# Performance work log

Measured on AMD Instinct MI355X. Metric: run time of the kernel, lower is better.

## Reference

```python
import jax, jax.numpy as jnp
import numpy as np

HEAD = 4
HW_DIM = 256  # in_dim // 2


def _gconv1x1(x, w, b):
    # groups=2 pointwise conv: x [B,C,H,W], w [O, C//2], b [O]
    B, C, H, W = x.shape
    O = w.shape[0]
    xg = x.reshape(B, 2, C // 2, H, W)
    wg = w.reshape(2, O // 2, C // 2)
    y = jnp.einsum('bgchw,goc->bgohw', xg, wg).reshape(B, O, H, W)
    return y + b[None, :, None, None]


def _bn_train(x, w, b, eps=1e-5):
    # BatchNorm2d in training mode (batch statistics over N,H,W)
    mean = x.mean(axis=(0, 2, 3), keepdims=True)
    var = ((x - mean) ** 2).mean(axis=(0, 2, 3), keepdims=True)
    return (x - mean) / jnp.sqrt(var + eps) * w[None, :, None, None] + b[None, :, None, None]


def _forward(x, wq, bq, wk, bk, wv, bv, bnh_w, bnh_b, bnw_w, bnw_b, gamma):
    B, C, H, W = x.shape
    org_x = x
    # first half of channels is detached in the original forward
    xd = jnp.concatenate([jax.lax.stop_gradient(x[:, :HW_DIM]), x[:, HW_DIM:]], axis=1)

    dqk_h = 512 // HEAD  # 128 per-head qk dim == `long`
    dv_h = 256 // HEAD   # 64 per-head value dim
    q = _gconv1x1(xd, wq, bq).reshape(B, HEAD, dqk_h, H, W)
    k = _gconv1x1(xd, wk, bk).reshape(B, HEAD, dqk_h, H, W)
    v = _gconv1x1(xd, wv, bv).reshape(B, HEAD, dv_h, H, W)
    scale = dqk_h ** (-0.5)

    # --- attention along H (per width column) ---
    eH = jnp.einsum('bnciw,bncjw->bnwij', q, k) * scale  # [B,HEAD,W,H,H]
    aH = jax.nn.softmax(eH, axis=-1)
    out_H = jnp.einsum('bnwij,bncjw->bnciw', aH, v).reshape(B, HEAD * dv_h, H, W)

    # --- attention along W (per height row) ---
    eW = jnp.einsum('bnchi,bnchj->bnhij', q, k) * scale  # [B,HEAD,H,W,W]
    aW = jax.nn.softmax(eW, axis=-1)
    out_W = jnp.einsum('bnhij,bnchj->bnchi', aW, v).reshape(B, HEAD * dv_h, H, W)

    p0 = _bn_train(out_H, bnh_w, bnh_b)[:, :HW_DIM // 2]
    p1 = _bn_train(out_W, bnw_w, bnw_b)[:, :HW_DIM // 2]

    out_temp = jnp.concatenate([out_H, out_W], axis=1)  # pre-BN outputs
    out = gamma * jax.nn.relu(out_temp) + org_x
    return out, p0, p1


def setup_inputs() -> dict:
    key = jax.random.key(0)
    ks = jax.random.split(key, 4)
    B, C, H, W = 4, 512, 128, 128
    s = 0.02
    return {
        'x': jax.random.normal(ks[0], (B, C, H, W), jnp.float32),
        'wq': jax.random.normal(ks[1], (512, 256), jnp.float32) * s,
        'bq': jnp.zeros((512,), jnp.float32),
        'wk': jax.random.normal(ks[2], (512, 256), jnp.float32) * s,
        'bk': jnp.zeros((512,), jnp.float32),
        'wv': jax.random.normal(ks[3], (256, 256), jnp.float32) * s,
        'bv': jnp.zeros((256,), jnp.float32),
        'bnh_w': jnp.ones((256,), jnp.float32),
        'bnh_b': jnp.zeros((256,), jnp.float32),
        'bnw_w': jnp.ones((256,), jnp.float32),
        'bnw_b': jnp.zeros((256,), jnp.float32),
        'gamma': jnp.full((1,), 0.1, jnp.float32),
    }


def reference(x, wq, bq, wk, bk, wv, bv, bnh_w, bnh_b, bnw_w, bnw_b, gamma):
    return _forward(x, wq, bq, wk, bk, wv, bv, bnh_w, bnh_b, bnw_w, bnw_b, gamma)
```

## Files before the change

### kernel.cpp

```cpp
#include <hip/hip_runtime.h>
#include <cstdint>
#include <cstddef>

constexpr int Bn = 4, Cin = 512, Hn = 128, Wn = 128, HWn = Hn * Wn;
constexpr float SCALE_LOG2E = 0.12751743f;
constexpr float INV_CNT = 1.52587890625e-05f;

typedef unsigned short u16;
typedef unsigned int u32;
using f32x4  = __attribute__((ext_vector_type(4))) float;
using bf16x8 = __attribute__((ext_vector_type(8))) short;

#define MFMA(a, b, c) __builtin_amdgcn_mfma_f32_16x16x32_bf16((a), (b), (c), 0, 0, 0)

__device__ __forceinline__ u16 bfu(float f) {
  u32 u = __float_as_uint(f);
  u += 0x7fffu + ((u >> 16) & 1u);
  return (u16)(u >> 16);
}

__device__ __forceinline__ void gload_lds16(const void* g, void* l) {
  __builtin_amdgcn_global_load_lds(
      (const __attribute__((address_space(1))) u32*)g,
      (__attribute__((address_space(3))) u32*)l, 16, 0, 0);
}

constexpr size_t SZ_XT = (size_t)Bn * HWn * 512 * 2;
constexpr size_t SZ_QK = (size_t)Bn * 4 * HWn * 128 * 2;
constexpr size_t SZ_V  = (size_t)Bn * 4 * HWn * 64 * 2;
constexpr size_t SZ_O  = (size_t)Bn * 256 * HWn * 4;
constexpr size_t OFF_XT = 0;
constexpr size_t OFF_Q  = OFF_XT + SZ_XT;
constexpr size_t OFF_K  = OFF_Q + SZ_QK;
constexpr size_t OFF_V  = OFF_K + SZ_QK;
constexpr size_t OFF_OH = OFF_V + SZ_V;
constexpr size_t OFF_OW = OFF_OH + SZ_O;
constexpr size_t OFF_ST = OFF_OW + SZ_O;
constexpr size_t OFF_WB = OFF_ST + 4096;
constexpr size_t OFF_BB = OFF_WB + (size_t)1280 * 256 * 2;

__global__ __launch_bounds__(256) void k_transpose_cast(
    const float* __restrict__ x,
    const float* __restrict__ wq, const float* __restrict__ wk, const float* __restrict__ wv,
    const float* __restrict__ bq, const float* __restrict__ bk, const float* __restrict__ bv,
    u16* __restrict__ xT, u16* __restrict__ Wb, float* __restrict__ Bb) {
  __shared__ float tile[32][33];
  const int t = threadIdx.x;
  if (blockIdx.z == 4) {
    if (blockIdx.y == 0 && blockIdx.x < 320) {
      int idx = (blockIdx.x * 256 + t) * 4;
      int row = idx >> 8, col = idx & 255;
      const float* src = (row < 512)  ? (wq + (size_t)row * 256 + col)
                       : (row < 1024) ? (wk + (size_t)(row - 512) * 256 + col)
                                      : (wv + (size_t)(row - 1024) * 256 + col);
      float4 v = *(const float4*)src;
      u32 lo = (u32)bfu(v.x) | ((u32)bfu(v.y) << 16);
      u32 hi = (u32)bfu(v.z) | ((u32)bfu(v.w) << 16);
      *(uint2*)&Wb[idx] = make_uint2(lo, hi);
    } else if (blockIdx.y == 1 && blockIdx.x == 0) {
      for (int i = t; i < 1280; i += 256)
        Bb[i] = (i < 512) ? bq[i] : (i < 1024) ? bk[i - 512] : bv[i - 1024];
    }
    return;
  }
  const int b = blockIdx.z, c0 = blockIdx.y * 32, p0 = blockIdx.x * 32;
  const int pi = t & 31, ci = t >> 5;
  const float* xp = x + ((size_t)b * Cin + c0) * HWn + p0;
  for (int cc = ci; cc < 32; cc += 8) tile[cc][pi] = xp[(size_t)cc * HWn + pi];
  __syncthreads();
  u16* o = xT + ((size_t)b * HWn + p0) * Cin + c0;
  for (int pp = ci; pp < 32; pp += 8) o[(size_t)pp * Cin + pi] = bfu(tile[pi][pp]);
}

__global__ __launch_bounds__(256, 3) void k_proj(
    const u16* __restrict__ xT, const u16* __restrict__ Wb, const float* __restrict__ Bb,
    u16* __restrict__ Q, u16* __restrict__ K, u16* __restrict__ V,
    float* __restrict__ stats) {
  __shared__ u16 xs[128 * 128];

  const int t = threadIdx.x;
  const int flat = blockIdx.x + 10 * (blockIdx.y + (blockIdx.z << 7));
  const int work = ((flat & 7) * 640) + (flat >> 3);
  const int ot = work % 10;
  const int rest = work / 10;
  const int b = rest >> 7;
  const int pos0 = (rest & 127) << 7;

  if (work == 0) { stats[t] = 0.f; stats[256 + t] = 0.f; }

  const int g = (ot < 8) ? ((ot & 3) >> 1) : (ot - 8);
  const u16* xrow = xT + ((size_t)b * HWn + pos0) * 512 + g * 256;

  const int lane = t & 63, wid = t >> 6, ln = lane & 15, qd = lane >> 4;
  const u16* wr0 = Wb + ((size_t)ot * 128 + wid * 32 + ln) * 256;

  f32x4 acc[2][8];
#pragma unroll
  for (int mi = 0; mi < 2; ++mi)
#pragma unroll
    for (int nt = 0; nt < 8; ++nt) acc[mi][nt] = f32x4{0.f, 0.f, 0.f, 0.f};

  for (int kc = 0; kc < 2; ++kc) {
    __syncthreads();
#pragma unroll
    for (int p = 0; p < 8; ++p) {
      int id = p * 256 + t;
      int pos = id >> 4, kb = id & 15;
      gload_lds16(xrow + (size_t)pos * 512 + kc * 128 + ((kb ^ (pos & 15)) << 3),
                  xs + id * 8);
    }
    bf16x8 a[2][4];
#pragma unroll
    for (int kk = 0; kk < 4; ++kk) {
      int kbi = kk * 4 + qd;
      a[0][kk] = *(const bf16x8*)(wr0 + kc * 128 + kbi * 8);
      a[1][kk] = *(const bf16x8*)(wr0 + 16 * 256 + kc * 128 + kbi * 8);
    }
    __syncthreads();
#pragma unroll
    for (int kk = 0; kk < 4; ++kk) {
      int kbi = kk * 4 + qd;
#pragma unroll
      for (int nt = 0; nt < 8; ++nt) {
        bf16x8 bf_ = *(const bf16x8*)(xs + (nt * 16 + ln) * 128 + (kbi ^ ln) * 8);
        acc[0][nt] = MFMA(a[0][kk], bf_, acc[0][nt]);
        acc[1][nt] = MFMA(a[1][kk], bf_, acc[1][nt]);
      }
    }
  }
  __syncthreads();
#pragma unroll
  for (int mi = 0; mi < 2; ++mi) {
    int oc = wid * 32 + mi * 16 + qd * 4;
    const float* bp = Bb + ot * 128 + oc;
    float b0 = bp[0], b1 = bp[1], b2 = bp[2], b3 = bp[3];
    int ocb = oc >> 2;
#pragma unroll
    for (int nt = 0; nt < 8; ++nt) {
      int pos = nt * 16 + ln;
      u32 lo = (u32)bfu(acc[mi][nt][0] + b0) | ((u32)bfu(acc[mi][nt][1] + b1) << 16);
      u32 hi = (u32)bfu(acc[mi][nt][2] + b2) | ((u32)bfu(acc[mi][nt][3] + b3) << 16);
      *(uint2*)&xs[pos * 128 + ((ocb ^ (pos & 31)) << 2)] = make_uint2(lo, hi);
    }
  }
  __syncthreads();
  if (ot < 8) {
    u16* dst = (ot < 4) ? Q + (size_t)(b * 4 + ot) * HWn * 128
                        : K + (size_t)(b * 4 + (ot - 4)) * HWn * 128;
#pragma unroll
    for (int p = 0; p < 8; ++p) {
      int id = p * 256 + t;
      int pos = id >> 4, grp = id & 15;
      int s0 = (grp * 2) ^ (pos & 31), s1 = (grp * 2 + 1) ^ (pos & 31);
      uint2 g0 = *(const uint2*)&xs[pos * 128 + (s0 << 2)];
      uint2 g1 = *(const uint2*)&xs[pos * 128 + (s1 << 2)];
      *(uint4*)(dst + (size_t)(pos0 + pos) * 128 + grp * 8) = make_uint4(g0.x, g0.y, g1.x, g1.y);
    }
  } else {
    u16* vb = V + (size_t)(b * 4 + (ot - 8) * 2) * HWn * 64;
#pragma unroll
    for (int p = 0; p < 8; ++p) {
      int id = p * 256 + t;
      int pos = id >> 4, grp = id & 15;
      int off = grp * 8;
      int s0 = (grp * 2) ^ (pos & 31), s1 = (grp * 2 + 1) ^ (pos & 31);
      uint2 g0 = *(const uint2*)&xs[pos * 128 + (s0 << 2)];
      uint2 g1 = *(const uint2*)&xs[pos * 128 + (s1 << 2)];
      u16* d = vb + (size_t)((off >> 6) * HWn + pos0 + pos) * 64 + (off & 63);
      *(uint4*)d = make_uint4(g0.x, g0.y, g1.x, g1.y);
    }
  }
}

__global__ __launch_bounds__(256, 3) void k_attn(
    const u16* __restrict__ Qg, const u16* __restrict__ Kg, const u16* __restrict__ Vg,
    const float* __restrict__ x, const float* __restrict__ gamma,
    float* __restrict__ outH, float* __restrict__ oWraw, float* __restrict__ out,
    float* __restrict__ stats) {
  __shared__ u16 sm[64 * 128 + 128 * 128];
  u16* VT = sm;
  u16* KP = sm + 64 * 128;
  float* scr = (float*)sm;

  const int t = threadIdx.x;
  const int s = blockIdx.x;
  const int b = blockIdx.y >> 2, n = blockIdx.y & 3;
  const int dir = blockIdx.z;
  const int pos_base = (dir == 0) ? s : s * 128;
  const int step = (dir == 0) ? 128 : 1;

  const u16* qb = Qg + (size_t)(b * 4 + n) * HWn * 128;
  const u16* kb = Kg + (size_t)(b * 4 + n) * HWn * 128;
  const u16* vb = Vg + (size_t)(b * 4 + n) * HWn * 64;

  const int lane = t & 63, wid = t >> 6, ln = lane & 15, qd = lane >> 4;

#pragma unroll
  for (int p = 0; p < 8; ++p) {
    int id = p * 256 + t;
    int row = id >> 4, kk = id & 15;
    gload_lds16(kb + (size_t)(pos_base + row * step) * 128 + ((kk ^ (row & 15)) << 3),
                KP + id * 8);
  }
  uint4 vreg[4];
#pragma unroll
  for (int p = 0; p < 4; ++p) {
    int id = p * 256 + t;
    int j = id >> 3, cb = id & 7;
    vreg[p] = *(const uint4*)(vb + (size_t)(pos_base + j * step) * 64 + cb * 8);
  }
  bf16x8 qa[2][4];
#pragma unroll
  for (int kk = 0; kk < 4; ++kk) {
    int kbi = kk * 4 + qd;
    qa[0][kk] = *(const bf16x8*)(qb + (size_t)(pos_base + (wid * 32 + ln) * step) * 128 + kbi * 8);
    qa[1][kk] = *(const bf16x8*)(qb + (size_t)(pos_base + (wid * 32 + 16 + ln) * step) * 128 + kbi * 8);
  }
#pragma unroll
  for (int p = 0; p < 4; ++p) {
    int id = p * 256 + t;
    int j = id >> 3, cb = id & 7;
    const u16* pv = (const u16*)&vreg[p];
    int jb = j >> 3, jr = j & 7;
#pragma unroll
    for (int e = 0; e < 8; ++e) {
      int c = cb * 8 + e;
      int sc = ((c >> 3) ^ c) & 15;
      VT[c * 128 + ((((jb ^ sc) & 15) << 3) | jr)] = pv[e];
    }
  }
  __syncthreads();

  f32x4 accS[2][8];
#pragma unroll
  for (int mi = 0; mi < 2; ++mi)
#pragma unroll
    for (int nt = 0; nt < 8; ++nt) accS[mi][nt] = f32x4{0.f, 0.f, 0.f, 0.f};

#pragma unroll
  for (int kk = 0; kk < 4; ++kk) {
    int kbi = kk * 4 + qd;
#pragma unroll
    for (int nt = 0; nt < 8; ++nt) {
      int row = nt * 16 + ln;
      bf16x8 bf_ = *(const bf16x8*)(KP + row * 128 + (kbi ^ ln) * 8);
      accS[0][nt] = MFMA(qa[0][kk], bf_, accS[0][nt]);
      accS[1][nt] = MFMA(qa[1][kk], bf_, accS[1][nt]);
    }
  }
  float rinv[2][4];
#pragma unroll
  for (int mi = 0; mi < 2; ++mi)
#pragma unroll
    for (int r = 0; r < 4; ++r) {
      float sum = 0.f;
#pragma unroll
      for (int nt = 0; nt < 8; ++nt) {
        float e = exp2f(accS[mi][nt][r] * SCALE_LOG2E);
        accS[mi][nt][r] = e; sum += e;
      }
      sum += __shfl_xor(sum, 1);
      sum += __shfl_xor(sum, 2);
      sum += __shfl_xor(sum, 4);
      sum += __shfl_xor(sum, 8);
      rinv[mi][r] = __builtin_amdgcn_rcpf(sum);
    }
  __syncthreads();
#pragma unroll
  for (int mi = 0; mi < 2; ++mi) {
    int mbase = (wid * 2 + mi) * 16 + qd * 4;
#pragma unroll
    for (int nt = 0; nt < 8; ++nt) {
      int nb = nt * 2 + (ln >> 3), nr = ln & 7;
#pragma unroll
      for (int r = 0; r < 4; ++r) {
        int m = mbase + r;
        KP[m * 128 + (((nb ^ (m & 15)) << 3) | nr)] = bfu(accS[mi][nt][r]);
      }
    }
  }
  f32x4 accO[2][4];
#pragma unroll
  for (int mi = 0; mi < 2; ++mi)
#pragma unroll
    for (int nt = 0; nt < 4; ++nt) accO[mi][nt] = f32x4{0.f, 0.f, 0.f, 0.f};
#pragma unroll
  for (int jj = 0; jj < 4; ++jj) {
    int jb2 = jj * 4 + qd;
    bf16x8 a0 = *(const bf16x8*)(KP + (wid * 32 + ln) * 128 + (jb2 ^ ln) * 8);
    bf16x8 a1 = *(const bf16x8*)(KP + (wid * 32 + 16 + ln) * 128 + (jb2 ^ ln) * 8);
#pragma unroll
    for (int nt = 0; nt < 4; ++nt) {
      int c = nt * 16 + ln;
      int sc = ((c >> 3) ^ c) & 15;
      bf16x8 bf_ = *(const bf16x8*)(VT + c * 128 + (((jb2 ^ sc) & 15) << 3));
      accO[0][nt] = MFMA(a0, bf_, accO[0][nt]);
      accO[1][nt] = MFMA(a1, bf_, accO[1][nt]);
    }
  }
  float s1[4] = {0.f, 0.f, 0.f, 0.f}, s2[4] = {0.f, 0.f, 0.f, 0.f};
  if (dir == 0) {
    float* obase = outH + ((size_t)(b * 4 + n) * 128 + s) * 8192;
#pragma unroll
    for (int mi = 0; mi < 2; ++mi) {
      int i0 = wid * 32 + mi * 16 + qd * 4;
#pragma unroll
      for (int nt = 0; nt < 4; ++nt) {
        int c = nt * 16 + ln;
        f32x4 v;
#pragma unroll
        for (int r = 0; r < 4; ++r) v[r] = accO[mi][nt][r] * rinv[mi][r];
        if (n < 2) {
#pragma unroll
          for (int r = 0; r < 4; ++r) { s1[nt] += v[r]; s2[nt] += v[r] * v[r]; }
        }
        *(f32x4*)(obase + (size_t)c * 128 + i0) = v;
      }
    }
  } else {
    const float gm = gamma[0];
    const float* xb = x + ((size_t)b * 512 + 256 + n * 64) * HWn + (size_t)s * 128;
    float* ob = out + ((size_t)b * 512 + 256 + n * 64) * HWn + (size_t)s * 128;
    float* rb = oWraw + ((size_t)b * 128 + n * 64) * HWn + (size_t)s * 128;
#pragma unroll
    for (int mi = 0; mi < 2; ++mi) {
      int i0 = wid * 32 + mi * 16 + qd * 4;
#pragma unroll
      for (int nt = 0; nt < 4; ++nt) {
        int c = nt * 16 + ln;
        f32x4 v;
#pragma unroll
        for (int r = 0; r < 4; ++r) v[r] = accO[mi][nt][r] * rinv[mi][r];
        if (n < 2) {
#pragma unroll
          for (int r = 0; r < 4; ++r) { s1[nt] += v[r]; s2[nt] += v[r] * v[r]; }
        }
        f32x4 xv = *(const f32x4*)(xb + (size_t)c * HWn + i0);
        f32x4 o;
#pragma unroll
        for (int r = 0; r < 4; ++r) o[r] = gm * fmaxf(v[r], 0.f) + xv[r];
        *(f32x4*)(ob + (size_t)c * HWn + i0) = o;
        if (n < 2) *(f32x4*)(rb + (size_t)c * HWn + i0) = v;
      }
    }
  }
  if (n < 2) {
    __syncthreads();
#pragma unroll
    for (int nt = 0; nt < 4; ++nt) {
      float a = s1[nt]; a += __shfl_xor(a, 16); a += __shfl_xor(a, 32);
      float q2 = s2[nt]; q2 += __shfl_xor(q2, 16); q2 += __shfl_xor(q2, 32);
      if (qd == 0) {
        scr[(wid * 2 + 0) * 64 + nt * 16 + ln] = a;
        scr[(wid * 2 + 1) * 64 + nt * 16 + ln] = q2;
      }
    }
    __syncthreads();
    if (t < 128) {
      int part = t >> 6, c2 = t & 63;
      float v = scr[part * 64 + c2] + scr[(2 + part) * 64 + c2] +
                scr[(4 + part) * 64 + c2] + scr[(6 + part) * 64 + c2];
      atomicAdd(&stats[dir * 256 + part * 128 + n * 64 + c2], v);
    }
  }
}

__global__ __launch_bounds__(256) void k_final(
    const float* __restrict__ x, const float* __restrict__ outH,
    const float* __restrict__ oWraw, const float* __restrict__ stats,
    const float* __restrict__ bnh_w, const float* __restrict__ bnh_b,
    const float* __restrict__ bnw_w, const float* __restrict__ bnw_b,
    const float* __restrict__ gamma,
    float* __restrict__ out, float* __restrict__ p0, float* __restrict__ p1) {
  __shared__ float lds[32 * 129];
  const int t = threadIdx.x;
  const int w0 = blockIdx.x * 32;
  const int ch = blockIdx.y;
  const int b = blockIdx.z;
  if (ch < 256) {
    const float gm = gamma[0];
    const float* xp = x + (size_t)(b * 512 + ch) * HWn;
    float* op = out + (size_t)(b * 512 + ch) * HWn;
    const int n = ch >> 6, c = ch & 63;
    const float* hb = outH + (size_t)(b * 4 + n) * 128 * 8192 + c * 128;
    for (int ps = 0; ps < 16; ++ps) {
      int wl = ps * 2 + (t >> 7);
      lds[wl * 129 + (t & 127)] = hb[(size_t)(w0 + wl) * 8192 + (t & 127)];
    }
    __syncthreads();
    const bool dop = ch < 128;
    float mean = 0.f, istd = 0.f, bw = 0.f, bb = 0.f;
    if (dop) {
      mean = stats[ch] * INV_CNT;
      float ex2 = stats[128 + ch] * INV_CNT;
      istd = rsqrtf(fmaxf(ex2 - mean * mean, 0.f) + 1e-5f);
      bw = bnh_w[ch]; bb = bnh_b[ch];
    }
    float* pp = p0 + (size_t)(b * 128 + ch) * HWn;
    const int w = t & 31, h0 = t >> 5;
    for (int hh = 0; hh < 16; ++hh) {
      int h = hh * 8 + h0;
      float v = lds[w * 129 + h];
      int gi = h * 128 + w0 + w;
      op[gi] = gm * fmaxf(v, 0.f) + xp[gi];
      if (dop) pp[gi] = (v - mean) * istd * bw + bb;
    }
  } else {
    const int cw = ch - 256;
    const float mean = stats[256 + cw] * INV_CNT;
    const float ex2 = stats[384 + cw] * INV_CNT;
    const float istd = rsqrtf(fmaxf(ex2 - mean * mean, 0.f) + 1e-5f);
    const float bw = bnw_w[cw], bb = bnw_b[cw];
    const float* rp = oWraw + (size_t)(b * 128 + cw) * HWn + (size_t)blockIdx.x * 4096;
    float* pp = p1 + (size_t)(b * 128 + cw) * HWn + (size_t)blockIdx.x * 4096;
#pragma unroll
    for (int it = 0; it < 4; ++it) {
      f32x4 v = *(const f32x4*)(rp + (it * 256 + t) * 4);
      f32x4 o;
#pragma unroll
      for (int r = 0; r < 4; ++r) o[r] = (v[r] - mean) * istd * bw + bb;
      *(f32x4*)(pp + (it * 256 + t) * 4) = o;
    }
  }
}

extern "C" void kernel_launch(void* const* d_in, const int* in_sizes, int n_in,
                              void* d_out, int out_size, void* d_ws, size_t ws_size,
                              hipStream_t stream) {
  (void)in_sizes; (void)n_in; (void)out_size; (void)ws_size;
  const float* x    = (const float*)d_in[0];
  const float* wq   = (const float*)d_in[1];
  const float* bq   = (const float*)d_in[2];
  const float* wk   = (const float*)d_in[3];
  const float* bk   = (const float*)d_in[4];
  const float* wv   = (const float*)d_in[5];
  const float* bv   = (const float*)d_in[6];
  const float* bnhw = (const float*)d_in[7];
  const float* bnhb = (const float*)d_in[8];
  const float* bnww = (const float*)d_in[9];
  const float* bnwb = (const float*)d_in[10];
  const float* gamma = (const float*)d_in[11];

  char* ws = (char*)d_ws;
  u16* xT = (u16*)(ws + OFF_XT);
  u16* Q  = (u16*)(ws + OFF_Q);
  u16* K  = (u16*)(ws + OFF_K);
  u16* V  = (u16*)(ws + OFF_V);
  float* oH = (float*)(ws + OFF_OH);
  float* oWr = (float*)(ws + OFF_OW);
  float* st = (float*)(ws + OFF_ST);
  u16* Wb = (u16*)(ws + OFF_WB);
  float* Bb = (float*)(ws + OFF_BB);

  float* out = (float*)d_out;
  float* p0 = out + (size_t)Bn * 512 * HWn;
  float* p1 = p0 + (size_t)Bn * 128 * HWn;

  k_transpose_cast<<<dim3(512, 16, 5), 256, 0, stream>>>(x, wq, wk, wv, bq, bk, bv, xT, Wb, Bb);
  k_proj<<<dim3(10, 128, 4), 256, 0, stream>>>(xT, Wb, Bb, Q, K, V, st);
  k_attn<<<dim3(128, 16, 2), 256, 0, stream>>>(Q, K, V, x, gamma, oH, oWr, out, st);
  k_final<<<dim3(4, 384, 4), 256, 0, stream>>>(x, oH, oWr, st, bnhw, bnhb, bnww, bnwb, gamma,
                                               out, p0, p1);
}
```

Baseline: 560.4 us.

## Compute transposed scores so P stays in registers, shrinking LDS for occupancy

```diff
diff --git a/kernel.cpp b/kernel.cpp
--- a/kernel.cpp
+++ b/kernel.cpp
@@ -10,6 +10,8 @@
 typedef unsigned int u32;
 using f32x4  = __attribute__((ext_vector_type(4))) float;
 using bf16x8 = __attribute__((ext_vector_type(8))) short;
+using s16x4  = __attribute__((ext_vector_type(4))) short;
+using u32x4  = __attribute__((ext_vector_type(4))) u32;
 
 #define MFMA(a, b, c) __builtin_amdgcn_mfma_f32_16x16x32_bf16((a), (b), (c), 0, 0, 0)
 
@@ -17,6 +19,9 @@
   u32 u = __float_as_uint(f);
   u += 0x7fffu + ((u >> 16) & 1u);
   return (u16)(u >> 16);
+}
+__device__ __forceinline__ u32 pk2(float a, float b) {
+  return (u32)bfu(a) | ((u32)bfu(b) << 16);
 }
 
 __device__ __forceinline__ void gload_lds16(const void* g, void* l) {
@@ -172,15 +177,14 @@
   }
 }
 
-__global__ __launch_bounds__(256, 3) void k_attn(
+__global__ __launch_bounds__(256, 4) void k_attn(
     const u16* __restrict__ Qg, const u16* __restrict__ Kg, const u16* __restrict__ Vg,
     const float* __restrict__ x, const float* __restrict__ gamma,
     float* __restrict__ outH, float* __restrict__ oWraw, float* __restrict__ out,
     float* __restrict__ stats) {
-  __shared__ u16 sm[64 * 128 + 128 * 128];
+  __shared__ u16 sm[128 * 128];
+  u16* KL = sm;
   u16* VT = sm;
-  u16* KP = sm + 64 * 128;
-  float* scr = (float*)sm;
 
   const int t = threadIdx.x;
   const int s = blockIdx.x;
@@ -200,7 +204,7 @@
     int id = p * 256 + t;
     int row = id >> 4, kk = id & 15;
     gload_lds16(kb + (size_t)(pos_base + row * step) * 128 + ((kk ^ (row & 15)) << 3),
-                KP + id * 8);
+                KL + id * 8);
   }
   uint4 vreg[4];
 #pragma unroll
@@ -209,13 +213,58 @@
     int j = id >> 3, cb = id & 7;
     vreg[p] = *(const uint4*)(vb + (size_t)(pos_base + j * step) * 64 + cb * 8);
   }
-  bf16x8 qa[2][4];
+  const u16* q0 = qb + (size_t)(pos_base + (size_t)(wid * 32 + ln) * step) * 128;
+  const u16* q1 = qb + (size_t)(pos_base + (size_t)(wid * 32 + 16 + ln) * step) * 128;
+  bf16x8 qc0 = *(const bf16x8*)(q0 + qd * 8);
+  bf16x8 qc1 = *(const bf16x8*)(q1 + qd * 8);
+  __syncthreads();
+
+  f32x4 accST[2][8];
+#pragma unroll
+  for (int nti = 0; nti < 2; ++nti)
+#pragma unroll
+    for (int mj = 0; mj < 8; ++mj) accST[nti][mj] = f32x4{0.f, 0.f, 0.f, 0.f};
 #pragma unroll
   for (int kk = 0; kk < 4; ++kk) {
     int kbi = kk * 4 + qd;
-    qa[0][kk] = *(const bf16x8*)(qb + (size_t)(pos_base + (wid * 32 + ln) * step) * 128 + kbi * 8);
-    qa[1][kk] = *(const bf16x8*)(qb + (size_t)(pos_base + (wid * 32 + 16 + ln) * step) * 128 + kbi * 8);
-  }
+    bf16x8 qn0 = qc0, qn1 = qc1;
+    if (kk < 3) {
+      qn0 = *(const bf16x8*)(q0 + (kbi + 4) * 8);
+      qn1 = *(const bf16x8*)(q1 + (kbi + 4) * 8);
+    }
+#pragma unroll
+    for (int mj = 0; mj < 8; ++mj) {
+      bf16x8 kf = *(const bf16x8*)(KL + (mj * 16 + ln) * 128 + ((kbi ^ ln) << 3));
+      accST[0][mj] = MFMA(kf, qc0, accST[0][mj]);
+      accST[1][mj] = MFMA(kf, qc1, accST[1][mj]);
+    }
+    qc0 = qn0; qc1 = qn1;
+  }
+
+  float rinv[2];
+  u32x4 pb[2][4];
+#pragma unroll
+  for (int nti = 0; nti < 2; ++nti) {
+    float sum = 0.f;
+#pragma unroll
+    for (int mj = 0; mj < 8; ++mj)
+#pragma unroll
+      for (int r = 0; r < 4; ++r) {
+        float e = exp2f(accST[nti][mj][r] * SCALE_LOG2E);
+        accST[nti][mj][r] = e; sum += e;
+      }
+    sum += __shfl_xor(sum, 16);
+    sum += __shfl_xor(sum, 32);
+    rinv[nti] = __builtin_amdgcn_rcpf(sum);
+#pragma unroll
+    for (int kk = 0; kk < 4; ++kk) {
+      pb[nti][kk][0] = pk2(accST[nti][kk * 2][0], accST[nti][kk * 2][1]);
+      pb[nti][kk][1] = pk2(accST[nti][kk * 2][2], accST[nti][kk * 2][3]);
+      pb[nti][kk][2] = pk2(accST[nti][kk * 2 + 1][0], accST[nti][kk * 2 + 1][1]);
+      pb[nti][kk][3] = pk2(accST[nti][kk * 2 + 1][2], accST[nti][kk * 2 + 1][3]);
+    }
+  }
+  __syncthreads();
 #pragma unroll
   for (int p = 0; p < 4; ++p) {
     int id = p * 256 + t;
@@ -231,91 +280,47 @@
   }
   __syncthreads();
 
-  f32x4 accS[2][8];
-#pragma unroll
-  for (int mi = 0; mi < 2; ++mi)
-#pragma unroll
-    for (int nt = 0; nt < 8; ++nt) accS[mi][nt] = f32x4{0.f, 0.f, 0.f, 0.f};
-
+  f32x4 accO[2][4];
+#pragma unroll
+  for (int nti = 0; nti < 2; ++nti)
+#pragma unroll
+    for (int ct = 0; ct < 4; ++ct) accO[nti][ct] = f32x4{0.f, 0.f, 0.f, 0.f};
 #pragma unroll
   for (int kk = 0; kk < 4; ++kk) {
-    int kbi = kk * 4 + qd;
-#pragma unroll
-    for (int nt = 0; nt < 8; ++nt) {
-      int row = nt * 16 + ln;
-      bf16x8 bf_ = *(const bf16x8*)(KP + row * 128 + (kbi ^ ln) * 8);
-      accS[0][nt] = MFMA(qa[0][kk], bf_, accS[0][nt]);
-      accS[1][nt] = MFMA(qa[1][kk], bf_, accS[1][nt]);
-    }
-  }
-  float rinv[2][4];
-#pragma unroll
-  for (int mi = 0; mi < 2; ++mi)
-#pragma unroll
-    for (int r = 0; r < 4; ++r) {
-      float sum = 0.f;
-#pragma unroll
-      for (int nt = 0; nt < 8; ++nt) {
-        float e = exp2f(accS[mi][nt][r] * SCALE_LOG2E);
-        accS[mi][nt][r] = e; sum += e;
-      }
-      sum += __shfl_xor(sum, 1);
-      sum += __shfl_xor(sum, 2);
-      sum += __shfl_xor(sum, 4);
-      sum += __shfl_xor(sum, 8);
-      rinv[mi][r] = __builtin_amdgcn_rcpf(sum);
-    }
-  __syncthreads();
-#pragma unroll
-  for (int mi = 0; mi < 2; ++mi) {
-    int mbase = (wid * 2 + mi) * 16 + qd * 4;
-#pragma unroll
-    for (int nt = 0; nt < 8; ++nt) {
-      int nb = nt * 2 + (ln >> 3), nr = ln & 7;
-#pragma unroll
-      for (int r = 0; r < 4; ++r) {
-        int m = mbase + r;
-        KP[m * 128 + (((nb ^ (m & 15)) << 3) | nr)] = bfu(accS[mi][nt][r]);
-      }
-    }
-  }
-  f32x4 accO[2][4];
-#pragma unroll
-  for (int mi = 0; mi < 2; ++mi)
-#pragma unroll
-    for (int nt = 0; nt < 4; ++nt) accO[mi][nt] = f32x4{0.f, 0.f, 0.f, 0.f};
-#pragma unroll
-  for (int jj = 0; jj < 4; ++jj) {
-    int jb2 = jj * 4 + qd;
-    bf16x8 a0 = *(const bf16x8*)(KP + (wid * 32 + ln) * 128 + (jb2 ^ ln) * 8);
-    bf16x8 a1 = *(const bf16x8*)(KP + (wid * 32 + 16 + ln) * 128 + (jb2 ^ ln) * 8);
-#pragma unroll
-    for (int nt = 0; nt < 4; ++nt) {
-      int c = nt * 16 + ln;
-      int sc = ((c >> 3) ^ c) & 15;
-      bf16x8 bf_ = *(const bf16x8*)(VT + c * 128 + (((jb2 ^ sc) & 15) << 3));
-      accO[0][nt] = MFMA(a0, bf_, accO[0][nt]);
-      accO[1][nt] = MFMA(a1, bf_, accO[1][nt]);
-    }
-  }
-  float s1[4] = {0.f, 0.f, 0.f, 0.f}, s2[4] = {0.f, 0.f, 0.f, 0.f};
+#pragma unroll
+    for (int ct = 0; ct < 4; ++ct) {
+      int crow = ct * 16 + ln;
+      int sc = ((crow >> 3) ^ crow) & 15;
+      int jbA = kk * 4 + (qd >> 1);
+      int off = (qd & 1) * 4;
+      const u16* vrow = VT + crow * 128;
+      s16x4 lo = *(const s16x4*)(vrow + (((jbA ^ sc) & 15) << 3) + off);
+      s16x4 hi = *(const s16x4*)(vrow + ((((jbA + 2) ^ sc) & 15) << 3) + off);
+      bf16x8 af = __builtin_shufflevector(lo, hi, 0, 1, 2, 3, 4, 5, 6, 7);
+      accO[0][ct] = MFMA(af, __builtin_bit_cast(bf16x8, pb[0][kk]), accO[0][ct]);
+      accO[1][ct] = MFMA(af, __builtin_bit_cast(bf16x8, pb[1][kk]), accO[1][ct]);
+    }
+  }
+
+  float bs1[4][4], bs2[4][4];
+#pragma unroll
+  for (int ct = 0; ct < 4; ++ct)
+#pragma unroll
+    for (int r = 0; r < 4; ++r) { bs1[ct][r] = 0.f; bs2[ct][r] = 0.f; }
+
   if (dir == 0) {
     float* obase = outH + ((size_t)(b * 4 + n) * 128 + s) * 8192;
 #pragma unroll
-    for (int mi = 0; mi < 2; ++mi) {
-      int i0 = wid * 32 + mi * 16 + qd * 4;
-#pragma unroll
-      for (int nt = 0; nt < 4; ++nt) {
-        int c = nt * 16 + ln;
-        f32x4 v;
-#pragma unroll
-        for (int r = 0; r < 4; ++r) v[r] = accO[mi][nt][r] * rinv[mi][r];
-        if (n < 2) {
-#pragma unroll
-          for (int r = 0; r < 4; ++r) { s1[nt] += v[r]; s2[nt] += v[r] * v[r]; }
+    for (int nti = 0; nti < 2; ++nti) {
+      int icol = wid * 32 + nti * 16 + ln;
+#pragma unroll
+      for (int ct = 0; ct < 4; ++ct)
+#pragma unroll
+        for (int r = 0; r < 4; ++r) {
+          float v = accO[nti][ct][r] * rinv[nti];
+          obase[(ct * 16 + qd * 4 + r) * 128 + icol] = v;
+          if (n < 2) { bs1[ct][r] += v; bs2[ct][r] += v * v; }
         }
-        *(f32x4*)(obase + (size_t)c * 128 + i0) = v;
-      }
     }
   } else {
     const float gm = gamma[0];
@@ -323,45 +328,34 @@
     float* ob = out + ((size_t)b * 512 + 256 + n * 64) * HWn + (size_t)s * 128;
     float* rb = oWraw + ((size_t)b * 128 + n * 64) * HWn + (size_t)s * 128;
 #pragma unroll
-    for (int mi = 0; mi < 2; ++mi) {
-      int i0 = wid * 32 + mi * 16 + qd * 4;
-#pragma unroll
-      for (int nt = 0; nt < 4; ++nt) {
-        int c = nt * 16 + ln;
-        f32x4 v;
-#pragma unroll
-        for (int r = 0; r < 4; ++r) v[r] = accO[mi][nt][r] * rinv[mi][r];
-        if (n < 2) {
-#pragma unroll
-          for (int r = 0; r < 4; ++r) { s1[nt] += v[r]; s2[nt] += v[r] * v[r]; }
+    for (int nti = 0; nti < 2; ++nti) {
+      int icol = wid * 32 + nti * 16 + ln;
+#pragma unroll
+      for (int ct = 0; ct < 4; ++ct)
+#pragma unroll
+        for (int r = 0; r < 4; ++r) {
+          float v = accO[nti][ct][r] * rinv[nti];
+          int c = ct * 16 + qd * 4 + r;
+          float xv = xb[(size_t)c * HWn + icol];
+          ob[(size_t)c * HWn + icol] = gm * fmaxf(v, 0.f) + xv;
+          if (n < 2) { rb[(size_t)c * HWn + icol] = v; bs1[ct][r] += v; bs2[ct][r] += v * v; }
         }
-        f32x4 xv = *(const f32x4*)(xb + (size_t)c * HWn + i0);
-        f32x4 o;
-#pragma unroll
-        for (int r = 0; r < 4; ++r) o[r] = gm * fmaxf(v[r], 0.f) + xv[r];
-        *(f32x4*)(ob + (size_t)c * HWn + i0) = o;
-        if (n < 2) *(f32x4*)(rb + (size_t)c * HWn + i0) = v;
+    }
+  }
+  if (n < 2) {
+#pragma unroll
+    for (int ct = 0; ct < 4; ++ct)
+#pragma unroll
+      for (int r = 0; r < 4; ++r) {
+        float a = bs1[ct][r], q = bs2[ct][r];
+        a += __shfl_xor(a, 1); a += __shfl_xor(a, 2); a += __shfl_xor(a, 4); a += __shfl_xor(a, 8);
+        q += __shfl_xor(q, 1); q += __shfl_xor(q, 2); q += __shfl_xor(q, 4); q += __shfl_xor(q, 8);
+        if (ln == 0) {
+          int c = ct * 16 + qd * 4 + r;
+          atomicAdd(&stats[dir * 256 + n * 64 + c], a);
+          atomicAdd(&stats[dir * 256 + 128 + n * 64 + c], q);
+        }
       }
-    }
-  }
-  if (n < 2) {
-    __syncthreads();
-#pragma unroll
-    for (int nt = 0; nt < 4; ++nt) {
-      float a = s1[nt]; a += __shfl_xor(a, 16); a += __shfl_xor(a, 32);
-      float q2 = s2[nt]; q2 += __shfl_xor(q2, 16); q2 += __shfl_xor(q2, 32);
-      if (qd == 0) {
-        scr[(wid * 2 + 0) * 64 + nt * 16 + ln] = a;
-        scr[(wid * 2 + 1) * 64 + nt * 16 + ln] = q2;
-      }
-    }
-    __syncthreads();
-    if (t < 128) {
-      int part = t >> 6, c2 = t & 63;
-      float v = scr[part * 64 + c2] + scr[(2 + part) * 64 + c2] +
-                scr[(4 + part) * 64 + c2] + scr[(6 + part) * 64 + c2];
-      atomicAdd(&stats[dir * 256 + part * 128 + n * 64 + c2], v);
-    }
   }
 }
 
```

New measurement: 814.6 us. +45.4%, slower.
